# Optimization experiments

Measured on AMD Instinct MI355X. Metric: run time of the kernel, lower is better.

The kernel has to match this reference:

```python
import jax, jax.numpy as jnp
import numpy as np
import math

G, NPG, D = 64, 2048, 128   # graphs, nodes per graph, feature dim
DEG = 16
N = G * NPG
E = N * DEG
VOCAB = 100000
RATIO = 0.8


def setup_inputs() -> dict:
    key = jax.random.key(0)
    ks = jax.random.split(key, 24)
    node_ids = jax.random.randint(ks[0], (N, 1), 0, VOCAB)
    # within-graph edges: endpoints in [0, NPG) per graph, then add graph offset
    within = jax.random.randint(ks[1], (2, G, NPG * DEG), 0, NPG)
    offs = (jnp.arange(G) * NPG)[None, :, None]
    edge_index = (within + offs).reshape(2, E)
    batch = jnp.repeat(jnp.arange(G), NPG)
    f = lambda k, shape: jax.random.normal(k, shape, dtype=jnp.float32) * 0.05
    return dict(
        node_ids=node_ids, edge_index=edge_index, batch=batch,
        emb=f(ks[2], (VOCAB, D)),
        Wl1=f(ks[3], (D, D)), Wr1=f(ks[4], (D, D)), bl1=f(ks[5], (D,)), pw1=f(ks[6], (D,)),
        Wl2=f(ks[7], (D, D)), Wr2=f(ks[8], (D, D)), bl2=f(ks[9], (D,)), pw2=f(ks[10], (D,)),
        Wl3=f(ks[11], (D, D)), Wr3=f(ks[12], (D, D)), bl3=f(ks[13], (D,)), pw3=f(ks[14], (D,)),
        W1=f(ks[15], (128, 256)), b1=f(ks[16], (128,)),
        W2=f(ks[17], (64, 128)), b2=f(ks[18], (64,)),
        W3=f(ks[19], (1, 64)), b3=f(ks[20], (1,)),
    )


def sage(x, src, dst, emask, Wl, bl, Wr):
    # PyG SAGEConv (mean aggr): lin_l(mean_j x_j) + lin_r(x_i); lin_r has no bias
    n = x.shape[0]
    msg = x[src] * emask[:, None].astype(x.dtype)
    dstm = jnp.where(emask, dst, n)  # dummy segment for invalid edges
    s = jax.ops.segment_sum(msg, dstm, num_segments=n + 1)[:n]
    c = jax.ops.segment_sum(emask.astype(x.dtype), dstm, num_segments=n + 1)[:n]
    mean = s / jnp.maximum(c, 1.0)[:, None]
    return mean @ Wl.T + bl + x @ Wr.T


def topk_pool(x, src, dst, emask, w, n_per):
    # PyG TopKPooling: score = tanh(x.w/||w||), keep top ceil(ratio*n) per graph,
    # scale kept features by score, remap/filter edges.
    n = x.shape[0]
    g = n // n_per
    k = math.ceil(RATIO * n_per)
    score = jnp.tanh((x @ w) / jnp.linalg.norm(w))
    ts, ti = jax.lax.top_k(score.reshape(g, n_per), k)  # [g, k]
    perm = (ti + (jnp.arange(g) * n_per)[:, None]).reshape(-1)  # old global idx
    x_new = x[perm] * ts.reshape(-1)[:, None]
    n_new = g * k
    new_of_old = jnp.full((n,), n_new, dtype=jnp.int32).at[perm].set(
        jnp.arange(n_new, dtype=jnp.int32))
    sn, dn = new_of_old[src], new_of_old[dst]
    em = emask & (sn < n_new) & (dn < n_new)
    sn = jnp.where(em, sn, 0)
    dn = jnp.where(em, dn, n_new)
    return x_new, sn, dn, em, k


def readout(x, k):
    # cat([global_max_pool, global_mean_pool]) with equal-size graphs
    g = x.shape[0] // k
    xr = x.reshape(g, k, -1)
    return jnp.concatenate([xr.max(axis=1), xr.mean(axis=1)], axis=1)


def reference(node_ids, edge_index, batch, emb,
              Wl1, Wr1, bl1, pw1, Wl2, Wr2, bl2, pw2, Wl3, Wr3, bl3, pw3,
              W1, b1, W2, b2, W3, b3):
    x = emb[node_ids.squeeze(1)]                       # [N, 128]
    src, dst = edge_index[0], edge_index[1]
    em = jnp.ones((src.shape[0],), dtype=bool)

    x = jax.nn.relu(sage(x, src, dst, em, Wl1, bl1, Wr1))
    x, src, dst, em, k1 = topk_pool(x, src, dst, em, pw1, NPG)
    x1 = readout(x, k1)

    x = jax.nn.relu(sage(x, src, dst, em, Wl2, bl2, Wr2))
    x, src, dst, em, k2 = topk_pool(x, src, dst, em, pw2, k1)
    x2 = readout(x, k2)

    x = jax.nn.relu(sage(x, src, dst, em, Wl3, bl3, Wr3))
    x, src, dst, em, k3 = topk_pool(x, src, dst, em, pw3, k2)
    x3 = readout(x, k3)

    h = x1 + x2 + x3                                   # [G, 256]
    h = jax.nn.relu(h @ W1.T + b1)
    h = jax.nn.relu(h @ W2.T + b2)                     # dropout = identity (eval)
    return jax.nn.sigmoid(h @ W3.T + b3).squeeze(1)    # [G]
```

## Files before the change

kernel.cpp:

```cpp
#include <hip/hip_runtime.h>
#include <hip/hip_bf16.h>
#include <float.h>

typedef _Float16 f16x8 __attribute__((ext_vector_type(8)));
typedef float f32x4 __attribute__((ext_vector_type(4)));

#define GRAPHS 64
#define NPG 2048
#define DIM 128
#define NNODES (GRAPHS * NPG)
#define NEDGES (NNODES * 16)
#define ECAP 32768
#define NSB 8
#define RSL 16
#define RPB 256

__global__ __launch_bounds__(256) void embed_kernel(const int* __restrict__ ids,
    const float* __restrict__ emb, _Float16* __restrict__ xh) {
  int idx = blockIdx.x * 256 + threadIdx.x;
  int nd = idx >> 4, part = idx & 15;
  int id = ids[nd];
  const float* src = emb + (size_t)id * 128 + part * 8;
  float4 a = *(const float4*)(src);
  float4 b = *(const float4*)(src + 4);
  f16x8 o;
  o[0] = (_Float16)a.x; o[1] = (_Float16)a.y; o[2] = (_Float16)a.z; o[3] = (_Float16)a.w;
  o[4] = (_Float16)b.x; o[5] = (_Float16)b.y; o[6] = (_Float16)b.z; o[7] = (_Float16)b.w;
  *(f16x8*)(xh + (size_t)nd * 128 + part * 8) = o;
}

__global__ __launch_bounds__(256) void convert_w3(const float* __restrict__ Wl0,
    const float* __restrict__ Wr0, const float* __restrict__ Wl1, const float* __restrict__ Wr1,
    const float* __restrict__ Wl2, const float* __restrict__ Wr2,
    _Float16* __restrict__ wh0, _Float16* __restrict__ wh1, _Float16* __restrict__ wh2) {
  int li = blockIdx.x >> 4;
  int qq = (blockIdx.x & 15) * 256 + threadIdx.x;
  const float* Wl = (li == 0) ? Wl0 : ((li == 1) ? Wl1 : Wl2);
  const float* Wr = (li == 0) ? Wr0 : ((li == 1) ? Wr1 : Wr2);
  _Float16* wh = (li == 0) ? wh0 : ((li == 1) ? wh1 : wh2);
  int ks = qq >> 9, nf = (qq >> 6) & 7, l = qq & 63;
  int ncol = nf * 16 + (l & 15);
  int k0 = (ks & 3) * 32 + ((l >> 4) << 3);
  const float* wsrc = ((ks < 4) ? Wl : Wr) + ncol * 128 + k0;
  float4 a = *(const float4*)wsrc;
  float4 b = *(const float4*)(wsrc + 4);
  f16x8 w;
  w[0] = (_Float16)a.x; w[1] = (_Float16)a.y; w[2] = (_Float16)a.z; w[3] = (_Float16)a.w;
  w[4] = (_Float16)b.x; w[5] = (_Float16)b.y; w[6] = (_Float16)b.z; w[7] = (_Float16)b.w;
  *(f16x8*)(wh + (size_t)qq * 8) = w;
}

__global__ __launch_bounds__(1024) void csr_hist(const int* __restrict__ src,
    const int* __restrict__ dst, int np, int* __restrict__ part) {
  __shared__ int hist[2048];
  int x = blockIdx.x;
  int s = x & 7, q = x >> 3;
  int b = q & (NSB - 1), gh = q >> 3;
  int g = gh * 8 + s;
  int tid = threadIdx.x;
  for (int i = tid; i < 2048; i += 1024) hist[i] = 0;
  __syncthreads();
  int e0 = g * ECAP + b * (ECAP / NSB);
  int nodebase = g * np;
  for (int e = tid; e < ECAP / NSB; e += 1024) {
    atomicAdd(&hist[dst[e0 + e] - nodebase], 1);
  }
  __syncthreads();
  for (int i = tid; i < np; i += 1024) part[((size_t)(g * NSB + b)) * 2048 + i] = hist[i];
}

__global__ __launch_bounds__(1024) void csr_scan(const int* __restrict__ part, int np,
    int* __restrict__ offb, int* __restrict__ deg, int* __restrict__ curs) {
  __shared__ int psum[1024];
  int g = blockIdx.x, tid = threadIdx.x;
  int i0 = 2 * tid, i1 = 2 * tid + 1;
  int p0[NSB], p1[NSB];
  int c0 = 0, c1 = 0;
#pragma unroll
  for (int b = 0; b < NSB; ++b) {
    p0[b] = (i0 < np) ? part[((size_t)(g * NSB + b)) * 2048 + i0] : 0;
    p1[b] = (i1 < np) ? part[((size_t)(g * NSB + b)) * 2048 + i1] : 0;
    c0 += p0[b]; c1 += p1[b];
  }
  int pair = c0 + c1;
  psum[tid] = pair;
  for (int s = 1; s < 1024; s <<= 1) {
    __syncthreads();
    int t = (tid >= s) ? psum[tid - s] : 0;
    __syncthreads();
    psum[tid] += t;
  }
  int excl = psum[tid] - pair;
  int ebase = g * ECAP;
  int nodebase = g * np;
  if (i0 < np) {
    int off = ebase + excl;
    offb[nodebase + i0] = off;
    deg[nodebase + i0] = c0;
    int cur = off;
#pragma unroll
    for (int b = 0; b < NSB; ++b) { curs[((size_t)(g * NSB + b)) * 2048 + i0] = cur; cur += p0[b]; }
  }
  if (i1 < np) {
    int off = ebase + excl + c0;
    offb[nodebase + i1] = off;
    deg[nodebase + i1] = c1;
    int cur = off;
#pragma unroll
    for (int b = 0; b < NSB; ++b) { curs[((size_t)(g * NSB + b)) * 2048 + i1] = cur; cur += p1[b]; }
  }
}

__global__ __launch_bounds__(1024) void csr_place(const int* __restrict__ src,
    const int* __restrict__ dst, int np, const int* __restrict__ curs,
    int* __restrict__ esort) {
  __shared__ int cur[2048];
  int x = blockIdx.x;
  int s = x & 7, q = x >> 3;
  int b = q & (NSB - 1), gh = q >> 3;
  int g = gh * 8 + s;
  int tid = threadIdx.x;
  for (int i = tid; i < np; i += 1024) cur[i] = curs[((size_t)(g * NSB + b)) * 2048 + i];
  __syncthreads();
  int e0 = g * ECAP + b * (ECAP / NSB);
  int nodebase = g * np;
  for (int e = tid; e < ECAP / NSB; e += 1024) {
    int ge = e0 + e;
    int p = atomicAdd(&cur[dst[ge] - nodebase], 1);
    esort[p] = src[ge];
  }
}

__global__ __launch_bounds__(256) void remap_esort(const int* __restrict__ esort0,
    const int* __restrict__ noo, int* __restrict__ esortl, int E4) {
  int t = blockIdx.x * 256 + threadIdx.x;
  if (t >= E4) return;
  int4 s = *(const int4*)(esort0 + t * 4);
  int4 o;
  o.x = noo[s.x]; o.y = noo[s.y]; o.z = noo[s.z]; o.w = noo[s.w];
  *(int4*)(esortl + t * 4) = o;
}

__global__ __launch_bounds__(256) void aggregate_kernel(const _Float16* __restrict__ xh,
    const int* __restrict__ offb, const int* __restrict__ deg, const int* __restrict__ esrc,
    _Float16* __restrict__ meanh, int np, int C) {
  int bid = blockIdx.x;
  int s = bid & 7, q = bid >> 3;
  int gsub = q / C, chunk = q - gsub * C;
  int g = gsub * 8 + s;
  int wave = threadIdx.x >> 6, lane = threadIdx.x & 63;
  int sub = lane >> 4, l = lane & 15;
  int local = chunk * 16 + wave * 4 + sub;
  if (local >= np) return;
  int w = g * np + local;
  int b = offb[w], c = deg[w];
  int e = b + c;
  float acc[8] = {0.f, 0.f, 0.f, 0.f, 0.f, 0.f, 0.f, 0.f};
  int i = b;
  for (; i + 4 <= e; i += 4) {
    int s0 = esrc[i], s1 = esrc[i + 1], s2 = esrc[i + 2], s3 = esrc[i + 3];
    f16x8 v0 = *(const f16x8*)(xh + (size_t)s0 * 128 + l * 8);
    f16x8 v1 = *(const f16x8*)(xh + (size_t)s1 * 128 + l * 8);
    f16x8 v2 = *(const f16x8*)(xh + (size_t)s2 * 128 + l * 8);
    f16x8 v3 = *(const f16x8*)(xh + (size_t)s3 * 128 + l * 8);
    f16x8 t = (v0 + v1) + (v2 + v3);
#pragma unroll
    for (int j = 0; j < 8; ++j) acc[j] += (float)t[j];
  }
  for (; i < e; ++i) {
    int srcn = esrc[i];
    f16x8 v = *(const f16x8*)(xh + (size_t)srcn * 128 + l * 8);
#pragma unroll
    for (int j = 0; j < 8; ++j) acc[j] += (float)v[j];
  }
  float inv = 1.f / (float)(c > 0 ? c : 1);
  f16x8 o;
#pragma unroll
  for (int j = 0; j < 8; ++j) o[j] = (_Float16)(acc[j] * inv);
  *(f16x8*)(meanh + (size_t)w * 128 + l * 8) = o;
}

__global__ __launch_bounds__(256) void aggregate_f(const _Float16* __restrict__ xh,
    const int* __restrict__ offb0, const int* __restrict__ deg0, const int* __restrict__ esortl,
    const int* __restrict__ orig, _Float16* __restrict__ meanh, int np, int C) {
  int bid = blockIdx.x;
  int s = bid & 7, q = bid >> 3;
  int gsub = q / C, chunk = q - gsub * C;
  int g = gsub * 8 + s;
  int wave = threadIdx.x >> 6, lane = threadIdx.x & 63;
  int sub = lane >> 4, l = lane & 15;
  int local = chunk * 16 + wave * 4 + sub;
  if (local >= np) return;
  int w = g * np + local;
  int o = orig[w];
  int b = offb0[o], c0 = deg0[o];
  int e = b + c0;
  float acc[8] = {0.f, 0.f, 0.f, 0.f, 0.f, 0.f, 0.f, 0.f};
  int cnt = 0;
  const f16x8 zero = {(_Float16)0.f, (_Float16)0.f, (_Float16)0.f, (_Float16)0.f,
                      (_Float16)0.f, (_Float16)0.f, (_Float16)0.f, (_Float16)0.f};
  int i = b;
  for (; i + 4 <= e; i += 4) {
    int n0 = esortl[i], n1 = esortl[i + 1], n2 = esortl[i + 2], n3 = esortl[i + 3];
    f16x8 v0 = zero, v1 = zero, v2 = zero, v3 = zero;
    if (n0 >= 0) v0 = *(const f16x8*)(xh + (size_t)n0 * 128 + l * 8);
    if (n1 >= 0) v1 = *(const f16x8*)(xh + (size_t)n1 * 128 + l * 8);
    if (n2 >= 0) v2 = *(const f16x8*)(xh + (size_t)n2 * 128 + l * 8);
    if (n3 >= 0) v3 = *(const f16x8*)(xh + (size_t)n3 * 128 + l * 8);
    cnt += (n0 >= 0) + (n1 >= 0) + (n2 >= 0) + (n3 >= 0);
    f16x8 t = (v0 + v1) + (v2 + v3);
#pragma unroll
    for (int j = 0; j < 8; ++j) acc[j] += (float)t[j];
  }
  for (; i < e; ++i) {
    int sn = esortl[i];
    if (sn < 0) continue;
    ++cnt;
    f16x8 v = *(const f16x8*)(xh + (size_t)sn * 128 + l * 8);
#pragma unroll
    for (int j = 0; j < 8; ++j) acc[j] += (float)v[j];
  }
  float inv = 1.f / (float)(cnt > 0 ? cnt : 1);
  f16x8 ov;
#pragma unroll
  for (int j = 0; j < 8; ++j) ov[j] = (_Float16)(acc[j] * inv);
  *(f16x8*)(meanh + (size_t)w * 128 + l * 8) = ov;
}

__global__ __launch_bounds__(256, 2) void sage_gemm(const _Float16* __restrict__ XH,
    const _Float16* MEANIN, _Float16* OUT, const _Float16* __restrict__ WH,
    const float* __restrict__ bl, const float* __restrict__ pw, float* __restrict__ sc,
    int n) {
  __shared__ _Float16 WB[4096 * 8];
  int tid = threadIdx.x;
  for (int qq = tid; qq < 4096; qq += 256)
    *(f16x8*)(WB + qq * 8) = *(const f16x8*)(WH + (size_t)qq * 8);
  __syncthreads();
  int wave = tid >> 6, lane = tid & 63;
  int wrow0 = blockIdx.x * RPB + wave * 64;
  if (wrow0 >= n) return;
  int kb = (lane >> 4) << 3;
  int lr = lane & 15;
  f32x4 acc[4][8];
#pragma unroll
  for (int t = 0; t < 4; ++t)
#pragma unroll
    for (int nf = 0; nf < 8; ++nf) acc[t][nf] = (f32x4){0.f, 0.f, 0.f, 0.f};
#pragma unroll
  for (int ks = 0; ks < 8; ++ks) {
    const _Float16* A = (ks < 4) ? MEANIN : XH;
    const _Float16* ap = A + (size_t)(wrow0 + lr) * 128 + (ks & 3) * 32 + kb;
    f16x8 a0 = *(const f16x8*)(ap);
    f16x8 a1 = *(const f16x8*)(ap + 16 * 128);
    f16x8 a2 = *(const f16x8*)(ap + 32 * 128);
    f16x8 a3 = *(const f16x8*)(ap + 48 * 128);
#pragma unroll
    for (int nf = 0; nf < 8; ++nf) {
      f16x8 b = *(const f16x8*)(WB + ((ks * 8 + nf) * 64 + lane) * 8);
      acc[0][nf] = __builtin_amdgcn_mfma_f32_16x16x32_f16(a0, b, acc[0][nf], 0, 0, 0);
      acc[1][nf] = __builtin_amdgcn_mfma_f32_16x16x32_f16(a1, b, acc[1][nf], 0, 0, 0);
      acc[2][nf] = __builtin_amdgcn_mfma_f32_16x16x32_f16(a2, b, acc[2][nf], 0, 0, 0);
      acc[3][nf] = __builtin_amdgcn_mfma_f32_16x16x32_f16(a3, b, acc[3][nf], 0, 0, 0);
    }
  }
  float pwv[8], qn = 0.f;
#pragma unroll
  for (int nf = 0; nf < 8; ++nf) {
    pwv[nf] = pw[nf * 16 + lr];
    qn += pwv[nf] * pwv[nf];
  }
#pragma unroll
  for (int o = 1; o < 16; o <<= 1) qn += __shfl_xor(qn, o);
  float inv_n = 1.f / sqrtf(qn);
#pragma unroll
  for (int t = 0; t < 4; ++t) {
    int rbase = wrow0 + t * 16 + ((lane >> 4) << 2);
    float dot[4] = {0.f, 0.f, 0.f, 0.f};
#pragma unroll
    for (int nf = 0; nf < 8; ++nf) {
      int col = nf * 16 + lr;
      float bias = bl[col];
#pragma unroll
      for (int r = 0; r < 4; ++r) {
        float v = fmaxf(acc[t][nf][r] + bias, 0.f);
        OUT[(size_t)(rbase + r) * 128 + col] = (_Float16)v;
        dot[r] += v * pwv[nf];
      }
    }
#pragma unroll
    for (int r = 0; r < 4; ++r) {
#pragma unroll
      for (int o = 1; o < 16; o <<= 1) dot[r] += __shfl_xor(dot[r], o);
    }
    if (lr == 0) {
#pragma unroll
      for (int r = 0; r < 4; ++r) sc[rbase + r] = tanhf(dot[r] * inv_n);
    }
  }
}

__global__ __launch_bounds__(1024) void topk_sort(const float* __restrict__ sc,
    int n_per, int k, int* __restrict__ nooA, int* __restrict__ rankt, int mode) {
  __shared__ unsigned long long L[2048];
  __shared__ int c2n[2048];
  int g = blockIdx.x;
  int tid = threadIdx.x;
  int lane = tid & 63, wave = tid >> 6;
  int i0 = wave * 128 + lane;
  int i1 = i0 + 64;
  const float* scg = sc + g * n_per;
  auto keyize = [&](int i) -> unsigned long long {
    float f = (i < n_per) ? scg[i] : -FLT_MAX;
    unsigned u = __float_as_uint(f);
    u = (u & 0x80000000u) ? ~u : (u | 0x80000000u);
    return ((unsigned long long)u << 32) | (unsigned)(2047 - i);
  };
  unsigned long long a = keyize(i0), b = keyize(i1);
#pragma clang loop unroll(disable)
  for (unsigned kk = 2; kk <= 2048; kk <<= 1) {
#pragma clang loop unroll(disable)
    for (unsigned j = kk >> 1; j >= 128; j >>= 1) {
      L[i0] = a; L[i1] = b;
      __syncthreads();
      unsigned long long pa = L[i0 ^ j], pb = L[i1 ^ j];
      bool dA = ((i0 & kk) == 0), lA = ((i0 & j) == 0);
      if ((dA == lA) ? (pa > a) : (pa < a)) a = pa;
      bool dB = ((i1 & kk) == 0), lB = ((i1 & j) == 0);
      if ((dB == lB) ? (pb > b) : (pb < b)) b = pb;
      __syncthreads();
    }
    if (kk >= 128) {
      bool desc = ((i0 & kk) == 0);
      if ((a < b) == desc) { unsigned long long t = a; a = b; b = t; }
    }
    unsigned jtop = (kk >> 1 < 32u) ? (kk >> 1) : 32u;
#pragma clang loop unroll(disable)
    for (unsigned j = jtop; j >= 1; j >>= 1) {
      unsigned long long oa = __shfl_xor(a, (int)j);
      unsigned long long ob = __shfl_xor(b, (int)j);
      bool low = ((lane & j) == 0);
      bool dA = ((i0 & kk) == 0);
      if ((dA == low) ? (oa > a) : (oa < a)) a = oa;
      bool dB = ((i1 & kk) == 0);
      if ((dB == low) ? (ob > b) : (ob < b)) b = ob;
    }
  }
  int orig_a = 2047 - (int)(a & 0xFFFFFFFFu);
  int orig_b = 2047 - (int)(b & 0xFFFFFFFFu);
  if (i0 < k) rankt[g * NPG + i0] = orig_a;
  if (i1 < k) rankt[g * NPG + i1] = orig_b;
  if (mode == 0) {
    if (orig_a < n_per) nooA[g * n_per + orig_a] = (i0 < k) ? g * k + i0 : -1;
    if (orig_b < n_per) nooA[g * n_per + orig_b] = (i1 < k) ? g * k + i1 : -1;
  } else if (mode == 1) {
    if (orig_a < n_per) c2n[orig_a] = (i0 < k) ? g * k + i0 : -1;
    if (orig_b < n_per) c2n[orig_b] = (i1 < k) ? g * k + i1 : -1;
    __syncthreads();
    for (int o2 = tid; o2 < NPG; o2 += 1024) {
      int a0 = nooA[g * NPG + o2];
      nooA[g * NPG + o2] = (a0 >= 0) ? c2n[a0 - g * n_per] : -1;
    }
  }
}

__global__ __launch_bounds__(256) void topk_tail(const float* __restrict__ sc,
    const int* __restrict__ rankt, int n_per, int k, const _Float16* __restrict__ meanin,
    _Float16* __restrict__ xh, const int* __restrict__ orig_in, int* __restrict__ orig_out,
    float* __restrict__ pmax, float* __restrict__ psum) {
  int g = blockIdx.x >> 4;
  int slice = blockIdx.x & (RSL - 1);
  int rpb = (k + RSL - 1) / RSL;
  int r0 = slice * rpb;
  int r1 = r0 + rpb; if (r1 > k) r1 = k;
  const float* scg = sc + g * n_per;
  int grp = threadIdx.x >> 4, l8 = threadIdx.x & 15;
  float vmax[8], vsum[8];
#pragma unroll
  for (int j = 0; j < 8; ++j) { vmax[j] = -FLT_MAX; vsum[j] = 0.f; }
  for (int r = r0 + grp; r < r1; r += 16) {
    int orig = rankt[g * NPG + r];
    int p = g * n_per + orig;
    float score = scg[orig];
    f16x8 v = *(const f16x8*)(meanin + (size_t)p * 128 + l8 * 8);
    f16x8 ovv;
#pragma unroll
    for (int j = 0; j < 8; ++j) {
      float val = (float)v[j] * score;
      ovv[j] = (_Float16)val;
      vmax[j] = fmaxf(vmax[j], val);
      vsum[j] += val;
    }
    *(f16x8*)(xh + (size_t)(g * k + r) * 128 + l8 * 8) = ovv;
    if (l8 == 0) orig_out[g * k + r] = orig_in ? orig_in[p] : p;
  }
  __shared__ float smax[4 * 128], ssum[4 * 128];
  int lane = threadIdx.x & 63, wave = threadIdx.x >> 6;
#pragma unroll
  for (int j = 0; j < 8; ++j) {
    vmax[j] = fmaxf(vmax[j], __shfl_xor(vmax[j], 16));
    vmax[j] = fmaxf(vmax[j], __shfl_xor(vmax[j], 32));
    vsum[j] += __shfl_xor(vsum[j], 16);
    vsum[j] += __shfl_xor(vsum[j], 32);
  }
  if ((lane >> 4) == 0) {
#pragma unroll
    for (int j = 0; j < 8; ++j) {
      smax[wave * 128 + l8 * 8 + j] = vmax[j];
      ssum[wave * 128 + l8 * 8 + j] = vsum[j];
    }
  }
  __syncthreads();
  if (threadIdx.x < 128) {
    int d = threadIdx.x;
    float m = fmaxf(fmaxf(smax[d], smax[128 + d]), fmaxf(smax[256 + d], smax[384 + d]));
    float s2 = ssum[d] + ssum[128 + d] + ssum[256 + d] + ssum[384 + d];
    pmax[(size_t)(g * RSL + slice) * 128 + d] = m;
    psum[(size_t)(g * RSL + slice) * 128 + d] = s2;
  }
}

__global__ __launch_bounds__(256) void mlp_fused(const float* __restrict__ pmax,
    const float* __restrict__ psum, int k0, int k1, int k2,
    const float* __restrict__ W1, const float* __restrict__ b1,
    const float* __restrict__ W2, const float* __restrict__ b2,
    const float* __restrict__ W3, const float* __restrict__ b3, float* __restrict__ out) {
  __shared__ float h[256], h1[128], h2[64];
  int g = blockIdx.x, t = threadIdx.x;
  int ks[3] = {k0, k1, k2};
  if (t < 128) {
    float hm = 0.f, hs = 0.f;
#pragma unroll
    for (int li = 0; li < 3; ++li) {
      const float* pm = pmax + ((size_t)li * GRAPHS + g) * RSL * 128;
      const float* ps = psum + ((size_t)li * GRAPHS + g) * RSL * 128;
      float m = -FLT_MAX, s = 0.f;
#pragma unroll
      for (int sl = 0; sl < RSL; ++sl) {
        m = fmaxf(m, pm[sl * 128 + t]);
        s += ps[sl * 128 + t];
      }
      hm += m;
      hs += s / (float)ks[li];
    }
    h[t] = hm;
    h[128 + t] = hs;
  }
  __syncthreads();
  if (t < 128) {
    const float* wp = W1 + t * 256;
    float a = b1[t];
    for (int c = 0; c < 256; ++c) a += h[c] * wp[c];
    h1[t] = fmaxf(a, 0.f);
  }
  __syncthreads();
  if (t < 64) {
    const float* wp = W2 + t * 128;
    float a = b2[t];
    for (int c = 0; c < 128; ++c) a += h1[c] * wp[c];
    h2[t] = fmaxf(a, 0.f);
  }
  __syncthreads();
  if (t < 64) {
    float a = h2[t] * W3[t];
#pragma unroll
    for (int o = 32; o >= 1; o >>= 1) a += __shfl_xor(a, o);
    if (t == 0) out[g] = 1.f / (1.f + expf(-(a + b3[0])));
  }
}

extern "C" void kernel_launch(void* const* d_in, const int* in_sizes, int n_in,
                              void* d_out, int out_size, void* d_ws, size_t ws_size,
                              hipStream_t stream) {
  const int* node_ids = (const int*)d_in[0];
  const int* ei = (const int*)d_in[1];
  const float* emb = (const float*)d_in[3];
  const float* W[3][4] = {
      {(const float*)d_in[4], (const float*)d_in[5], (const float*)d_in[6], (const float*)d_in[7]},
      {(const float*)d_in[8], (const float*)d_in[9], (const float*)d_in[10], (const float*)d_in[11]},
      {(const float*)d_in[12], (const float*)d_in[13], (const float*)d_in[14], (const float*)d_in[15]}};
  const float* W1 = (const float*)d_in[16];
  const float* b1 = (const float*)d_in[17];
  const float* W2 = (const float*)d_in[18];
  const float* b2 = (const float*)d_in[19];
  const float* W3 = (const float*)d_in[20];
  const float* b3 = (const float*)d_in[21];
  float* out = (float*)d_out;

  const int E = NEDGES;
  char* ws = (char*)d_ws;
  size_t o = 0;
  auto alloc = [&](size_t bytes) { void* p = ws + o; o = (o + bytes + 255) & ~(size_t)255; return p; };
  _Float16* XH = (_Float16*)alloc((size_t)NNODES * 128 * 2);
  _Float16* MEANH = (_Float16*)alloc((size_t)NNODES * 128 * 2);
  int* ESORT = (int*)alloc((size_t)E * 4);
  int* ESORTL = (int*)alloc((size_t)E * 4);
  int* PART = (int*)alloc((size_t)GRAPHS * NSB * 2048 * 4);
  int* CURS = (int*)alloc((size_t)GRAPHS * NSB * 2048 * 4);
  int* OFFB = (int*)alloc((size_t)NNODES * 4);
  int* DEG = (int*)alloc((size_t)NNODES * 4);
  float* SC = (float*)alloc((size_t)NNODES * 4);
  int* NOOA = (int*)alloc((size_t)NNODES * 4);
  int* RANKT = (int*)alloc((size_t)NNODES * 4);
  int* ORIGA = (int*)alloc((size_t)NNODES * 4);
  int* ORIGB = (int*)alloc((size_t)NNODES * 4);
  _Float16* WH0 = (_Float16*)alloc(4096 * 8 * 2);
  _Float16* WH1 = (_Float16*)alloc(4096 * 8 * 2);
  _Float16* WH2 = (_Float16*)alloc(4096 * 8 * 2);
  float* PMAX = (float*)alloc((size_t)3 * GRAPHS * RSL * 128 * 4);
  float* PSUM = (float*)alloc((size_t)3 * GRAPHS * RSL * 128 * 4);

  embed_kernel<<<NNODES * 16 / 256, 256, 0, stream>>>(node_ids, emb, XH);
  convert_w3<<<48, 256, 0, stream>>>(W[0][0], W[0][1], W[1][0], W[1][1], W[2][0], W[2][1],
                                     WH0, WH1, WH2);

  const int* src = ei;
  const int* dst = ei + E;
  csr_hist<<<GRAPHS * NSB, 1024, 0, stream>>>(src, dst, NPG, PART);
  csr_scan<<<GRAPHS, 1024, 0, stream>>>(PART, NPG, OFFB, DEG, CURS);
  csr_place<<<GRAPHS * NSB, 1024, 0, stream>>>(src, dst, NPG, CURS, ESORT);

  struct LayerP { int n, k; };
  LayerP L[3] = {{131072, 1639}, {104896, 1312}, {83968, 1050}};
  _Float16* WHs[3] = {WH0, WH1, WH2};
  int* ORIG_cur = ORIGA;
  int* ORIG_next = ORIGB;

  for (int li = 0; li < 3; ++li) {
    int n = L[li].n, k = L[li].k;
    int np = n / 64;
    const float *bl = W[li][2], *pw = W[li][3];

    int C = (np + 15) / 16;
    if (li == 0) {
      aggregate_kernel<<<64 * C, 256, 0, stream>>>(XH, OFFB, DEG, ESORT, MEANH, np, C);
    } else {
      remap_esort<<<E / 4 / 256, 256, 0, stream>>>(ESORT, NOOA, ESORTL, E / 4);
      aggregate_f<<<64 * C, 256, 0, stream>>>(XH, OFFB, DEG, ESORTL, ORIG_cur,
                                              MEANH, np, C);
    }
    sage_gemm<<<(n + RPB - 1) / RPB, 256, 0, stream>>>(XH, MEANH, MEANH, WHs[li], bl, pw, SC, n);
    topk_sort<<<GRAPHS, 1024, 0, stream>>>(SC, np, k, NOOA, RANKT, li);
    topk_tail<<<GRAPHS * RSL, 256, 0, stream>>>(SC, RANKT, np, k, MEANH, XH,
        (li == 0) ? nullptr : ORIG_cur, ORIG_next,
        PMAX + (size_t)li * GRAPHS * RSL * 128, PSUM + (size_t)li * GRAPHS * RSL * 128);
    { int* t = ORIG_cur; ORIG_cur = ORIG_next; ORIG_next = t; }
  }

  mlp_fused<<<GRAPHS, 256, 0, stream>>>(PMAX, PSUM, L[0].k, L[1].k, L[2].k,
                                        W1, b1, W2, b2, W3, b3, out);
}
```

Before: 331.6 us.

## Fuse edge-source remap into topk_sort and enlarge sage_gemm blocks to 512 threads

Drops the standalone remap_esort kernel. Each topk_sort block now builds an old-to-new node map for its graph in shared memory and rewrites that graph's slice of the CSR source array, which removes a launch and the random global lookups into the node map. Mode 1 keeps the composed map in shared memory and no longer writes nooA back to global. Separately, sage_gemm moves to 512-thread blocks with 512 rows each, so fewer blocks each stage the weight matrix into shared memory, at the cost of fewer resident blocks. The remap work now runs inside 64 blocks, which may serialize it on fewer CUs.

```diff
diff --git a/kernel.cpp b/kernel.cpp
--- a/kernel.cpp
+++ b/kernel.cpp
@@ -13,7 +13,7 @@
 #define ECAP 32768
 #define NSB 8
 #define RSL 16
-#define RPB 256
+#define RPB 512
 
 __global__ __launch_bounds__(256) void embed_kernel(const int* __restrict__ ids,
     const float* __restrict__ emb, _Float16* __restrict__ xh) {
@@ -129,16 +129,6 @@
     int p = atomicAdd(&cur[dst[ge] - nodebase], 1);
     esort[p] = src[ge];
   }
-}
-
-__global__ __launch_bounds__(256) void remap_esort(const int* __restrict__ esort0,
-    const int* __restrict__ noo, int* __restrict__ esortl, int E4) {
-  int t = blockIdx.x * 256 + threadIdx.x;
-  if (t >= E4) return;
-  int4 s = *(const int4*)(esort0 + t * 4);
-  int4 o;
-  o.x = noo[s.x]; o.y = noo[s.y]; o.z = noo[s.z]; o.w = noo[s.w];
-  *(int4*)(esortl + t * 4) = o;
 }
 
 __global__ __launch_bounds__(256) void aggregate_kernel(const _Float16* __restrict__ xh,
@@ -227,13 +217,13 @@
   *(f16x8*)(meanh + (size_t)w * 128 + l * 8) = ov;
 }
 
-__global__ __launch_bounds__(256, 2) void sage_gemm(const _Float16* __restrict__ XH,
+__global__ __launch_bounds__(512) void sage_gemm(const _Float16* __restrict__ XH,
     const _Float16* MEANIN, _Float16* OUT, const _Float16* __restrict__ WH,
     const float* __restrict__ bl, const float* __restrict__ pw, float* __restrict__ sc,
     int n) {
   __shared__ _Float16 WB[4096 * 8];
   int tid = threadIdx.x;
-  for (int qq = tid; qq < 4096; qq += 256)
+  for (int qq = tid; qq < 4096; qq += 512)
     *(f16x8*)(WB + qq * 8) = *(const f16x8*)(WH + (size_t)qq * 8);
   __syncthreads();
   int wave = tid >> 6, lane = tid & 63;
@@ -300,9 +290,11 @@
 }
 
 __global__ __launch_bounds__(1024) void topk_sort(const float* __restrict__ sc,
-    int n_per, int k, int* __restrict__ nooA, int* __restrict__ rankt, int mode) {
+    int n_per, int k, int* __restrict__ nooA, int* __restrict__ rankt,
+    const int* __restrict__ esort0, int* __restrict__ esortl, int mode) {
   __shared__ unsigned long long L[2048];
   __shared__ int c2n[2048];
+  int* comp = (int*)L;
   int g = blockIdx.x;
   int tid = threadIdx.x;
   int lane = tid & 63, wave = tid >> 6;
@@ -350,15 +342,29 @@
   if (i0 < k) rankt[g * NPG + i0] = orig_a;
   if (i1 < k) rankt[g * NPG + i1] = orig_b;
   if (mode == 0) {
-    if (orig_a < n_per) nooA[g * n_per + orig_a] = (i0 < k) ? g * k + i0 : -1;
-    if (orig_b < n_per) nooA[g * n_per + orig_b] = (i1 < k) ? g * k + i1 : -1;
+    int na = (i0 < k) ? g * k + i0 : -1;
+    int nb = (i1 < k) ? g * k + i1 : -1;
+    nooA[g * n_per + orig_a] = na;
+    nooA[g * n_per + orig_b] = nb;
+    c2n[orig_a] = na;
+    c2n[orig_b] = nb;
+    __syncthreads();
+    for (int e = tid; e < ECAP; e += 1024) {
+      int v = esort0[g * ECAP + e];
+      esortl[g * ECAP + e] = c2n[v - g * NPG];
+    }
   } else if (mode == 1) {
     if (orig_a < n_per) c2n[orig_a] = (i0 < k) ? g * k + i0 : -1;
     if (orig_b < n_per) c2n[orig_b] = (i1 < k) ? g * k + i1 : -1;
     __syncthreads();
     for (int o2 = tid; o2 < NPG; o2 += 1024) {
       int a0 = nooA[g * NPG + o2];
-      nooA[g * NPG + o2] = (a0 >= 0) ? c2n[a0 - g * n_per] : -1;
+      comp[o2] = (a0 >= 0) ? c2n[a0 - g * n_per] : -1;
+    }
+    __syncthreads();
+    for (int e = tid; e < ECAP; e += 1024) {
+      int v = esort0[g * ECAP + e];
+      esortl[g * ECAP + e] = comp[v - g * NPG];
     }
   }
 }
@@ -534,12 +540,11 @@
     if (li == 0) {
       aggregate_kernel<<<64 * C, 256, 0, stream>>>(XH, OFFB, DEG, ESORT, MEANH, np, C);
     } else {
-      remap_esort<<<E / 4 / 256, 256, 0, stream>>>(ESORT, NOOA, ESORTL, E / 4);
       aggregate_f<<<64 * C, 256, 0, stream>>>(XH, OFFB, DEG, ESORTL, ORIG_cur,
                                               MEANH, np, C);
     }
-    sage_gemm<<<(n + RPB - 1) / RPB, 256, 0, stream>>>(XH, MEANH, MEANH, WHs[li], bl, pw, SC, n);
-    topk_sort<<<GRAPHS, 1024, 0, stream>>>(SC, np, k, NOOA, RANKT, li);
+    sage_gemm<<<(n + RPB - 1) / RPB, 512, 0, stream>>>(XH, MEANH, MEANH, WHs[li], bl, pw, SC, n);
+    topk_sort<<<GRAPHS, 1024, 0, stream>>>(SC, np, k, NOOA, RANKT, ESORT, ESORTL, li);
     topk_tail<<<GRAPHS * RSL, 256, 0, stream>>>(SC, RANKT, np, k, MEANH, XH,
         (li == 0) ? nullptr : ORIG_cur, ORIG_next,
         PMAX + (size_t)li * GRAPHS * RSL * 128, PSUM + (size_t)li * GRAPHS * RSL * 128);
```

After: 317.6 us. 4.2% less time.
